# Optimization experiments

Hardware: AMD Instinct MI355X
Metric: run time of the kernel (lower is better)

Reference implementation:

```python
import jax, jax.numpy as jnp
import numpy as np

B, N, F_IN, F_OUT = 8, 2048, 128, 64
ALPHA = 0.2  # LeakyReLU negative slope
NEG_INF = -9e15


def setup_inputs() -> dict:
    key = jax.random.key(0)
    k1, k2, k3, k4 = jax.random.split(key, 4)
    h = jax.random.normal(k1, (B, N, F_IN), dtype=jnp.float32)
    adj = jax.random.randint(k2, (B, N, N), 0, 2, dtype=jnp.int32)
    # xavier_uniform with gain=1.414 approximated by scaled normals (values are arbitrary params)
    W = jax.random.normal(k3, (F_IN, F_OUT), dtype=jnp.float32) * (1.414 * np.sqrt(2.0 / (F_IN + F_OUT)))
    a = jax.random.normal(k4, (2 * F_OUT, 1), dtype=jnp.float32) * (1.414 * np.sqrt(2.0 / (2 * F_OUT + 1)))
    return {"h": h, "adj": adj, "W": W, "a": a}


def reference(h, adj, W, a):
    # Wh: [B, N, F_out]
    Wh = jnp.einsum('bnf,fo->bno', h, W)
    Fo = W.shape[1]
    a1 = a[:Fo, 0]   # [F_out]
    a2 = a[Fo:, 0]   # [F_out]
    # e[b,i,j] = leakyrelu(Wh[b,i]@a1 + Wh[b,j]@a2)  (== cat(Wh_i,Wh_j)@a, same math, no N^2*2F blowup)
    e1 = jnp.einsum('bno,o->bn', Wh, a1)  # [B, N]
    e2 = jnp.einsum('bno,o->bn', Wh, a2)  # [B, N]
    e = e1[:, :, None] + e2[:, None, :]   # [B, N, N]
    e = jnp.where(e > 0, e, ALPHA * e)    # LeakyReLU
    e = jnp.where(adj > 0, e, NEG_INF)    # mask non-edges
    attention = jax.nn.softmax(e, axis=-1)
    # dropout is identity in inference mode (deterministic reference)
    h_prime = jnp.einsum('bij,bjo->bio', attention, Wh)  # [B, N, F_out]
    return jax.nn.elu(h_prime)  # concat=True branch
```

## Files before the change

### kernel.cpp

```cpp
#include <hip/hip_runtime.h>
#include <hip/hip_bf16.h>

#define BB 8
#define NN 2048
#define FIN 128
#define FO 64
#define ALPHA 0.2f

typedef __attribute__((ext_vector_type(8))) short bf16x8;
typedef __attribute__((ext_vector_type(4))) float f32x4;
typedef __attribute__((ext_vector_type(4))) int i32x4;

typedef __attribute__((address_space(1))) const void gvoid;
typedef __attribute__((address_space(3))) void lvoid;

__device__ inline void gl_lds16(const void* g, void* l) {
    __builtin_amdgcn_global_load_lds((gvoid*)g, (lvoid*)l, 16, 0, 0);
}

__device__ inline short f2bf(float x) {
    unsigned u = __float_as_uint(x);
    u += 0x7fffu + ((u >> 16) & 1u);
    return (short)(u >> 16);
}

__global__ __launch_bounds__(256) void wh_kernel(
    const float* __restrict__ h, const float* __restrict__ W,
    const float* __restrict__ a, float* __restrict__ e1, float* __restrict__ e2,
    short* __restrict__ whF)
{
    __shared__ float hs[32][FIN];
    const int r0 = blockIdx.x * 32;
    const int t = threadIdx.x;
    const float4* hsrc = (const float4*)(h + (size_t)r0 * FIN);
    float4* hdst = (float4*)(&hs[0][0]);
#pragma unroll
    for (int k = 0; k < 4; k++) hdst[t + 256 * k] = hsrc[t + 256 * k];
    __syncthreads();

    const int o = t & 63;
    const int wv = t >> 6;
    float acc[8];
#pragma unroll
    for (int rr = 0; rr < 8; rr++) acc[rr] = 0.f;

    for (int f = 0; f < FIN; f += 4) {
        const float w0 = W[(f + 0) * FO + o];
        const float w1 = W[(f + 1) * FO + o];
        const float w2 = W[(f + 2) * FO + o];
        const float w3 = W[(f + 3) * FO + o];
#pragma unroll
        for (int rr = 0; rr < 8; rr++) {
            float4 hv = *(const float4*)&hs[wv * 8 + rr][f];
            acc[rr] = fmaf(hv.x, w0, acc[rr]);
            acc[rr] = fmaf(hv.y, w1, acc[rr]);
            acc[rr] = fmaf(hv.z, w2, acc[rr]);
            acc[rr] = fmaf(hv.w, w3, acc[rr]);
        }
    }

    const int b   = r0 / NN;
    const int ib0 = r0 - b * NN;
    const int ibb = ib0 + wv * 8;
    const int jc  = ibb >> 5;
    const int qq  = (ibb >> 3) & 3;
    const int ot  = o >> 4, mm = o & 15;
    const int L   = mm + qq * 16;
    bf16x8 frag;
#pragma unroll
    for (int rr = 0; rr < 8; rr++) frag[rr] = f2bf(acc[rr]);
    *(bf16x8*)(whF + ((((size_t)(b * 64 + jc) * 4 + ot) * 64 + L) * 8)) = frag;

    const float a1 = a[o], a2 = a[FO + o];
#pragma unroll
    for (int rr = 0; rr < 8; rr++) {
        float v1 = acc[rr] * a1, v2 = acc[rr] * a2;
#pragma unroll
        for (int msk = 32; msk >= 1; msk >>= 1) {
            v1 += __shfl_xor(v1, msk, 64);
            v2 += __shfl_xor(v2, msk, 64);
        }
        if (o == 0) { e1[r0 + wv * 8 + rr] = v1; e2[r0 + wv * 8 + rr] = v2; }
    }
}

__global__ __launch_bounds__(256) void e2max_kernel(
    const float* __restrict__ e2, float* __restrict__ e2max)
{
    const int b = blockIdx.x;
    const int t = threadIdx.x;
    float m = -1e30f;
    for (int j = t; j < NN; j += 256) m = fmaxf(m, e2[b * NN + j]);
#pragma unroll
    for (int k = 32; k >= 1; k >>= 1) m = fmaxf(m, __shfl_xor(m, k, 64));
    __shared__ float red[4];
    if ((t & 63) == 0) red[t >> 6] = m;
    __syncthreads();
    if (t == 0) e2max[b] = fmaxf(fmaxf(red[0], red[1]), fmaxf(red[2], red[3]));
}

struct SMemS {
    int   adjs[4][4][16][8][4];
    float e2s[4][512];
};
struct SMemC { float comb[4][16][64]; float lsum[4][16]; };
union SMemU { SMemS s; SMemC c; };

#define WAITVM_(n) asm volatile("s_waitcnt vmcnt(" #n ")" ::: "memory")
#define WAITVM(n) WAITVM_(n)

#define STAGE(k) do { \
    gl_lds16(asrc0 + (size_t)(k) * 32, &ladj[(k) & 3][0][0][0]); \
    gl_lds16(asrc1 + (size_t)(k) * 32, &ladj[(k) & 3][8][0][0]); \
} while (0)

#define STEPC(k, VM) do { \
    WAITVM(VM); \
    i32x4 va0 = *(const i32x4*)&ladj[(k) & 3][m][u0][0]; \
    i32x4 va1 = *(const i32x4*)&ladj[(k) & 3][m][u1][0]; \
    f32x4 ev0 = *(const f32x4*)&le2[(k) * 32 + q * 8]; \
    f32x4 ev1 = *(const f32x4*)&le2[(k) * 32 + q * 8 + 4]; \
    const short* bfp = whFw + (size_t)(k) * 2048; \
    bf16x8 wb0 = *(const bf16x8*)(bfp); \
    bf16x8 wb1 = *(const bf16x8*)(bfp + 512); \
    bf16x8 wb2 = *(const bf16x8*)(bfp + 1024); \
    bf16x8 wb3 = *(const bf16x8*)(bfp + 1536); \
    float pe[8]; \
    _Pragma("unroll") \
    for (int jj = 0; jj < 8; jj++) { \
        const int   av = (jj < 4) ? va0[jj] : va1[jj - 4]; \
        const float ej = (jj < 4) ? ev0[jj] : ev1[jj - 4]; \
        const float s  = fmaf(ej, L2E, E1v); \
        const float tt = fmaf(ALPHA, fminf(s, 0.f), fmaxf(s, 0.f)) - MiB; \
        pe[jj] = __builtin_amdgcn_exp2f(fmaf((float)av, 4000.0f, tt)); \
    } \
    union { unsigned u[4]; bf16x8 v; } au; \
    _Pragma("unroll") \
    for (int jj = 0; jj < 4; jj++) \
        au.u[jj] = __builtin_amdgcn_perm(__float_as_uint(pe[2 * jj + 1]), \
                                         __float_as_uint(pe[2 * jj]), 0x07060302u); \
    acc0 = __builtin_amdgcn_mfma_f32_16x16x32_bf16(au.v, wb0, acc0, 0, 0, 0); \
    acc1 = __builtin_amdgcn_mfma_f32_16x16x32_bf16(au.v, wb1, acc1, 0, 0, 0); \
    acc2 = __builtin_amdgcn_mfma_f32_16x16x32_bf16(au.v, wb2, acc2, 0, 0, 0); \
    acc3 = __builtin_amdgcn_mfma_f32_16x16x32_bf16(au.v, wb3, acc3, 0, 0, 0); \
    acc4 = __builtin_amdgcn_mfma_f32_16x16x32_bf16(au.v, ones, acc4, 0, 0, 0); \
} while (0)

__global__ __launch_bounds__(256, 4) void attn_kernel(
    const int* __restrict__ adj, const float* __restrict__ e1,
    const float* __restrict__ e2, const float* __restrict__ e2max,
    const short* __restrict__ whF, float* __restrict__ out)
{
    __shared__ __align__(16) SMemU sm;
    const int t = threadIdx.x, w = t >> 6, lane = t & 63;
    const int m = lane & 15, q = lane >> 4;
    const int blk = blockIdx.x;
    const int b = blk >> 7, i0 = (blk & 127) * 16;

    const float L2E = 1.4426950408889634f;
    const float e1v = e1[b * NN + i0 + m];
    float mr = e1v + e2max[b];
    mr = mr > 0.f ? mr : ALPHA * mr;
    const float E1v = e1v * L2E;
    const float MiB = mr * L2E + 4000.0f;

    const int l8 = lane >> 3, c7 = lane & 7;
    const int csw = (c7 ^ l8) * 4;
    const int* asrc0 = adj + ((size_t)(b * NN + i0 + l8)) * NN + w * 512 + csw;
    const int* asrc1 = asrc0 + (size_t)8 * NN;
    int (*ladj)[16][8][4] = sm.s.adjs[w];
    float* le2 = sm.s.e2s[w];
    const float* e2src = e2 + b * NN + w * 512 + lane * 4;

    const short* whFw = whF + (size_t)b * (64 * 4 * 64 * 8)
                            + (size_t)(w * 16) * 2048 + lane * 8;

    f32x4 acc0 = {0.f,0.f,0.f,0.f}, acc1 = acc0, acc2 = acc0, acc3 = acc0, acc4 = acc0;
    bf16x8 ones;
#pragma unroll
    for (int jj = 0; jj < 8; jj++) ones[jj] = (short)0x3F80;

    const int u0 = (q * 2) ^ (m & 7);
    const int u1 = u0 ^ 1;

    gl_lds16(e2src,       &le2[0]);
    gl_lds16(e2src + 256, &le2[256]);
    STAGE(0); STAGE(1); STAGE(2);

#pragma unroll 1
    for (int k = 0; k < 13; k++) {
        STAGE(k + 3);
        STEPC(k, 6);
    }
    STEPC(13, 4);
    STEPC(14, 2);
    STEPC(15, 0);

    __syncthreads();
    if (m == 0) {
#pragma unroll
        for (int r = 0; r < 4; r++) sm.c.lsum[w][q * 4 + r] = acc4[r];
    }
#pragma unroll
    for (int ot = 0; ot < 4; ot++) {
        f32x4 av = (ot == 0) ? acc0 : (ot == 1) ? acc1 : (ot == 2) ? acc2 : acc3;
#pragma unroll
        for (int reg = 0; reg < 4; reg++)
            sm.c.comb[w][q * 4 + reg][ot * 16 + m] = av[reg];
    }
    __syncthreads();

    const int row = t >> 4, c0 = (t & 15) * 4;
    f32x4 sum = *(const f32x4*)&sm.c.comb[0][row][c0];
#pragma unroll
    for (int ww = 1; ww < 4; ww++) {
        f32x4 sv = *(const f32x4*)&sm.c.comb[ww][row][c0];
        sum.x += sv.x; sum.y += sv.y; sum.z += sv.z; sum.w += sv.w;
    }
    float l = sm.c.lsum[0][row] + sm.c.lsum[1][row] + sm.c.lsum[2][row] + sm.c.lsum[3][row];
    l = fmaxf(l, 1e-30f);
    const float rl = 1.f / l;
    f32x4 res;
    float vr[4] = { sum.x * rl, sum.y * rl, sum.z * rl, sum.w * rl };
#pragma unroll
    for (int kk = 0; kk < 4; kk++)
        res[kk] = vr[kk] > 0.f ? vr[kk] : (__expf(vr[kk]) - 1.f);
    *(f32x4*)&out[((size_t)(b * NN + i0 + row)) * FO + c0] = res;
}

extern "C" void kernel_launch(void* const* d_in, const int* in_sizes, int n_in,
                              void* d_out, int out_size, void* d_ws, size_t ws_size,
                              hipStream_t stream) {
    const float* h   = (const float*)d_in[0];
    const int*   adj = (const int*)d_in[1];
    const float* W   = (const float*)d_in[2];
    const float* a   = (const float*)d_in[3];
    float* out = (float*)d_out;

    char* ws = (char*)d_ws;
    short* whF = (short*)ws;
    size_t off = (size_t)BB * 64 * 4 * 64 * 8 * sizeof(short);
    float* e1  = (float*)(ws + off);  off += (size_t)BB * NN * 4;
    float* e2  = (float*)(ws + off);  off += (size_t)BB * NN * 4;
    float* e2m = (float*)(ws + off);

    wh_kernel<<<(BB * NN) / 32, 256, 0, stream>>>(h, W, a, e1, e2, whF);
    e2max_kernel<<<BB, 256, 0, stream>>>(e2, e2m);
    attn_kernel<<<BB * (NN / 16), 256, 0, stream>>>(adj, e1, e2, e2m, whF, out);
}
```

Measured before the change: 222.3 us.

## Prefetch Wh fragments two steps ahead and rebalance vmcnt waits

Global loads of the Wh B-fragments are software-pipelined two iterations ahead in register-held WFrag structs, and the loop is unrolled by two. The s_waitcnt vmcnt thresholds are recomputed so the adjacency LDS stages and the prefetched register loads overlap. This targets the global-load latency exposed when the fragments were loaded inside each step. The LeakyReLU is simplified to max(s, alpha*s) with a pre-negated bias, and the occupancy hint is dropped from launch_bounds, which raises register pressure and may lower occupancy.

```diff
diff --git a/kernel.cpp b/kernel.cpp
--- a/kernel.cpp
+++ b/kernel.cpp
@@ -106,47 +106,55 @@
 struct SMemC { float comb[4][16][64]; float lsum[4][16]; };
 union SMemU { SMemS s; SMemC c; };
 
+struct WFrag { bf16x8 f0, f1, f2, f3; };
+
+#define CFENCE asm volatile("" ::: "memory")
 #define WAITVM_(n) asm volatile("s_waitcnt vmcnt(" #n ")" ::: "memory")
 #define WAITVM(n) WAITVM_(n)
 
 #define STAGE(k) do { \
     gl_lds16(asrc0 + (size_t)(k) * 32, &ladj[(k) & 3][0][0][0]); \
     gl_lds16(asrc1 + (size_t)(k) * 32, &ladj[(k) & 3][8][0][0]); \
+    CFENCE; \
 } while (0)
 
-#define STEPC(k, VM) do { \
+#define WLOAD(dst, k) do { \
+    const short* bfp = whFw + (size_t)(k) * 2048; \
+    dst.f0 = *(const bf16x8*)(bfp); \
+    dst.f1 = *(const bf16x8*)(bfp + 512); \
+    dst.f2 = *(const bf16x8*)(bfp + 1024); \
+    dst.f3 = *(const bf16x8*)(bfp + 1536); \
+    CFENCE; \
+} while (0)
+
+#define STEPC(k, VM, WF) do { \
     WAITVM(VM); \
     i32x4 va0 = *(const i32x4*)&ladj[(k) & 3][m][u0][0]; \
     i32x4 va1 = *(const i32x4*)&ladj[(k) & 3][m][u1][0]; \
     f32x4 ev0 = *(const f32x4*)&le2[(k) * 32 + q * 8]; \
     f32x4 ev1 = *(const f32x4*)&le2[(k) * 32 + q * 8 + 4]; \
-    const short* bfp = whFw + (size_t)(k) * 2048; \
-    bf16x8 wb0 = *(const bf16x8*)(bfp); \
-    bf16x8 wb1 = *(const bf16x8*)(bfp + 512); \
-    bf16x8 wb2 = *(const bf16x8*)(bfp + 1024); \
-    bf16x8 wb3 = *(const bf16x8*)(bfp + 1536); \
     float pe[8]; \
     _Pragma("unroll") \
     for (int jj = 0; jj < 8; jj++) { \
         const int   av = (jj < 4) ? va0[jj] : va1[jj - 4]; \
         const float ej = (jj < 4) ? ev0[jj] : ev1[jj - 4]; \
         const float s  = fmaf(ej, L2E, E1v); \
-        const float tt = fmaf(ALPHA, fminf(s, 0.f), fmaxf(s, 0.f)) - MiB; \
-        pe[jj] = __builtin_amdgcn_exp2f(fmaf((float)av, 4000.0f, tt)); \
+        const float lk = fmaxf(s, ALPHA * s); \
+        pe[jj] = __builtin_amdgcn_exp2f(lk + fmaf((float)av, 4000.0f, negMiB)); \
     } \
     union { unsigned u[4]; bf16x8 v; } au; \
     _Pragma("unroll") \
     for (int jj = 0; jj < 4; jj++) \
         au.u[jj] = __builtin_amdgcn_perm(__float_as_uint(pe[2 * jj + 1]), \
                                          __float_as_uint(pe[2 * jj]), 0x07060302u); \
-    acc0 = __builtin_amdgcn_mfma_f32_16x16x32_bf16(au.v, wb0, acc0, 0, 0, 0); \
-    acc1 = __builtin_amdgcn_mfma_f32_16x16x32_bf16(au.v, wb1, acc1, 0, 0, 0); \
-    acc2 = __builtin_amdgcn_mfma_f32_16x16x32_bf16(au.v, wb2, acc2, 0, 0, 0); \
-    acc3 = __builtin_amdgcn_mfma_f32_16x16x32_bf16(au.v, wb3, acc3, 0, 0, 0); \
+    acc0 = __builtin_amdgcn_mfma_f32_16x16x32_bf16(au.v, WF.f0, acc0, 0, 0, 0); \
+    acc1 = __builtin_amdgcn_mfma_f32_16x16x32_bf16(au.v, WF.f1, acc1, 0, 0, 0); \
+    acc2 = __builtin_amdgcn_mfma_f32_16x16x32_bf16(au.v, WF.f2, acc2, 0, 0, 0); \
+    acc3 = __builtin_amdgcn_mfma_f32_16x16x32_bf16(au.v, WF.f3, acc3, 0, 0, 0); \
     acc4 = __builtin_amdgcn_mfma_f32_16x16x32_bf16(au.v, ones, acc4, 0, 0, 0); \
 } while (0)
 
-__global__ __launch_bounds__(256, 4) void attn_kernel(
+__global__ __launch_bounds__(256) void attn_kernel(
     const int* __restrict__ adj, const float* __restrict__ e1,
     const float* __restrict__ e2, const float* __restrict__ e2max,
     const short* __restrict__ whF, float* __restrict__ out)
@@ -162,7 +170,7 @@
     float mr = e1v + e2max[b];
     mr = mr > 0.f ? mr : ALPHA * mr;
     const float E1v = e1v * L2E;
-    const float MiB = mr * L2E + 4000.0f;
+    const float negMiB = -(mr * L2E + 4000.0f);
 
     const int l8 = lane >> 3, c7 = lane & 7;
     const int csw = (c7 ^ l8) * 4;
@@ -185,16 +193,20 @@
 
     gl_lds16(e2src,       &le2[0]);
     gl_lds16(e2src + 256, &le2[256]);
+    CFENCE;
     STAGE(0); STAGE(1); STAGE(2);
+    WFrag W0f, W1f;
+    WLOAD(W0f, 0); WLOAD(W1f, 1);
 
 #pragma unroll 1
-    for (int k = 0; k < 13; k++) {
-        STAGE(k + 3);
-        STEPC(k, 6);
-    }
-    STEPC(13, 4);
-    STEPC(14, 2);
-    STEPC(15, 0);
+    for (int k = 0; k < 12; k += 2) {
+        WFrag Wa; WLOAD(Wa, k + 2); STAGE(k + 3); STEPC(k, 18, W0f); W0f = Wa;
+        WFrag Wb; WLOAD(Wb, k + 3); STAGE(k + 4); STEPC(k + 1, 18, W1f); W1f = Wb;
+    }
+    { WFrag Wa; WLOAD(Wa, 14); STAGE(15); STEPC(12, 18, W0f); W0f = Wa; }
+    { WFrag Wb; WLOAD(Wb, 15);            STEPC(13, 16, W1f); W1f = Wb; }
+    STEPC(14, 10, W0f);
+    STEPC(15,  4, W1f);
 
     __syncthreads();
     if (m == 0) {
```

Measured after the change: 220.0 us. Within noise of the previous version (-1.1%).
